# Kernel optimization log

Measured on AMD Instinct MI355X. Metric: run time of the kernel, lower is better.

The kernel has to match this reference:

```python
import jax, jax.numpy as jnp
import numpy as np

N, M, B, C, L, H = 8192, 8192, 16, 512, 64, 8
HEAD_DIM = C // H
PER_BATCH_KEYS = M // B
MASK_VAL = -1000.0  # matches torch masked_fill_ value


def setup_inputs() -> dict:
    key0 = jax.random.key(0)
    ks = jax.random.split(key0, 8)
    query = jax.random.normal(ks[0], (N, C), jnp.float32)
    key = jax.random.normal(ks[1], (M, C), jnp.float32)
    value = jax.random.normal(ks[2], (M, C), jnp.float32)
    # xavier-ish init for projections
    in_proj_weight = jax.random.normal(ks[3], (3 * C, C), jnp.float32) * (1.0 / np.sqrt(C))
    in_proj_bias = jnp.zeros((3 * C,), jnp.float32)
    out_w = jax.random.normal(ks[4], (C, C), jnp.float32) * (1.0 / np.sqrt(C))
    out_b = jnp.zeros((C,), jnp.float32)
    index_pair = jax.random.randint(ks[5], (N, L), 0, PER_BATCH_KEYS).astype(jnp.int32)
    pad = jax.random.uniform(ks[6], (N, L)) < 0.05
    index_pair = jnp.where(pad, jnp.int32(-1), index_pair)
    query_batch_cnt = jnp.full((B,), N // B, jnp.int32)
    key_batch_cnt = jnp.full((B,), PER_BATCH_KEYS, jnp.int32)
    index_pair_batch = jnp.repeat(jnp.arange(B, dtype=jnp.int32), N // B)
    return {
        "query": query, "key": key, "value": value,
        "in_proj_weight": in_proj_weight, "in_proj_bias": in_proj_bias,
        "out_w": out_w, "out_b": out_b,
        "index_pair": index_pair, "query_batch_cnt": query_batch_cnt,
        "key_batch_cnt": key_batch_cnt, "index_pair_batch": index_pair_batch,
    }


def reference(query, key, value, in_proj_weight, in_proj_bias, out_w, out_b,
              index_pair, query_batch_cnt, key_batch_cnt, index_pair_batch):
    embed_dim = query.shape[-1]
    scaling = float(HEAD_DIM) ** -0.5
    # qkv projections (in_proj_weight is [3C, C], applied as F.linear => x @ W.T + b)
    q = (query @ in_proj_weight[:embed_dim].T + in_proj_bias[:embed_dim]) * scaling
    k = key @ in_proj_weight[embed_dim:2 * embed_dim].T + in_proj_bias[embed_dim:2 * embed_dim]
    v = value @ in_proj_weight[2 * embed_dim:].T + in_proj_bias[2 * embed_dim:]
    q = q.reshape(N, H, HEAD_DIM)
    k = k.reshape(M, H, HEAD_DIM)
    v = v.reshape(M, H, HEAD_DIM)
    # local -> global key indices: offset by start of each query's batch key block
    key_start = jnp.cumsum(key_batch_cnt) - key_batch_cnt          # (B,)
    offset = key_start[index_pair_batch]                            # (N,)
    valid = index_pair >= 0                                         # (N, L)
    gidx = jnp.where(valid, index_pair + offset[:, None], 0)        # (N, L), safe gather
    # gather-based scores: (N, L, H)
    scores = jnp.einsum("nhd,nlhd->nlh", q, k[gidx])
    scores = jnp.where(valid[..., None], scores, MASK_VAL)
    w = jax.nn.softmax(scores, axis=1)                              # softmax over neighbors L
    # weighted value sum; masked weights underflow to exactly 0 in fp32
    attn = jnp.einsum("nlh,nlhd->nhd", w, v[gidx]).reshape(N, embed_dim)
    attn = attn @ out_w.T + out_b
    return attn, w.sum(axis=-1) / H
```

## Files before the change

### kernel.cpp

```cpp
#include <hip/hip_runtime.h>
#include <hip/hip_bf16.h>
#include <math.h>

#define NQ 8192
#define MK 8192
#define CD 512
#define LN 64
#define HH 8
#define HD 64
#define BB 16
#define KPB 512
#define QPB 512

typedef short short8 __attribute__((ext_vector_type(8)));
typedef float floatx4 __attribute__((ext_vector_type(4)));

__device__ __forceinline__ unsigned short f2bf(float x) {
    unsigned int u = __builtin_bit_cast(unsigned int, x);
    return (unsigned short)((u + 0x7FFFu + ((u >> 16) & 1u)) >> 16);
}
__device__ __forceinline__ unsigned int pkbf(float lo, float hi) {
    float2 f; f.x = lo; f.y = hi;
    __hip_bfloat162 h2 = __float22bfloat162_rn(f);
    unsigned int u;
    __builtin_memcpy(&u, &h2, 4);
    return u;
}
__device__ __forceinline__ float bflo(unsigned int u) {
    return __builtin_bit_cast(float, u << 16);
}
__device__ __forceinline__ float bfhij(unsigned int u) {
    return __builtin_bit_cast(float, u);
}
__device__ __forceinline__ short8 u4s8(uint4 u) {
    short8 s; __builtin_memcpy(&s, &u, 16); return s;
}
__device__ __forceinline__ float exp2v(float x) {
    float r; asm("v_exp_f32 %0, %1" : "=v"(r) : "v"(x)); return r;
}
__device__ __forceinline__ float rcpv(float x) {
    float r; asm("v_rcp_f32 %0, %1" : "=v"(r) : "v"(x)); return r;
}

__device__ __forceinline__ void gl_lds16(const unsigned short* g, unsigned short* l) {
    __builtin_amdgcn_global_load_lds(
        (const __attribute__((address_space(1))) unsigned int*)g,
        (__attribute__((address_space(3))) unsigned int*)l, 16, 0, 0);
}

struct ConvSeg { const float* src; unsigned short* dst; int n4; };
struct ConvArgs { ConvSeg s[5]; };

__global__ __launch_bounds__(256) void convert_bf16(ConvArgs a) {
    const int seg = blockIdx.y;
    const int i = blockIdx.x * 256 + threadIdx.x;
    if (i >= a.s[seg].n4) return;
    const float4 v = ((const float4*)a.s[seg].src)[i];
    uint2 o; o.x = pkbf(v.x, v.y); o.y = pkbf(v.z, v.w);
    ((uint2*)a.s[seg].dst)[i] = o;
}

template<int MI>
__device__ __forceinline__ void gemm_bf_body(const unsigned short* __restrict__ A,
                                             const unsigned short* __restrict__ W,
                                             const float* __restrict__ bias,
                                             float* __restrict__ outf,
                                             unsigned short* __restrict__ outb,
                                             float scale) {
    __shared__ unsigned short As[MI * 16 * 64];
    __shared__ unsigned short Bs[128 * 64];

    const int tid  = threadIdx.x;
    const int row0 = blockIdx.x * (MI * 16);
    const int col0 = blockIdx.y * 128;

    const int w    = tid >> 6;
    const int lane = tid & 63;
    const int q    = lane >> 4;
    const int ml   = lane & 15;

    const int sr = lane >> 3;
    const int sg = (lane & 7) ^ sr;
    const unsigned short* Ap = A + (size_t)(row0 + w * (MI * 4) + sr) * CD + sg * 8;
    const unsigned short* Wp = W + (size_t)(col0 + w * 32 + sr) * CD + sg * 8;
    unsigned short* Asw = &As[(w * (MI * 4)) * 64];
    unsigned short* Bsw = &Bs[(w * 32) * 64];

    floatx4 acc[MI][2];
#pragma unroll
    for (int i = 0; i < MI; ++i)
#pragma unroll
        for (int j = 0; j < 2; ++j)
            acc[i][j] = (floatx4){0.f, 0.f, 0.f, 0.f};

    for (int k0 = 0; k0 < CD; k0 += 64) {
        __syncthreads();
#pragma unroll
        for (int i = 0; i < MI / 2; ++i)
            gl_lds16(Ap + (size_t)(i * 8) * CD + k0, Asw + i * 8 * 64);
#pragma unroll
        for (int i = 0; i < 4; ++i)
            gl_lds16(Wp + (size_t)(i * 8) * CD + k0, Bsw + i * 8 * 64);
        __syncthreads();

#pragma unroll
        for (int kw = 0; kw < 2; ++kw) {
            short8 af[MI], bf[2];
            const int gp = ((kw * 4 + q) ^ (ml & 7)) * 8;
#pragma unroll
            for (int mi = 0; mi < MI; ++mi)
                af[mi] = *(const short8*)&As[(mi * 16 + ml) * 64 + gp];
#pragma unroll
            for (int ni = 0; ni < 2; ++ni)
                bf[ni] = *(const short8*)&Bs[(w * 32 + ni * 16 + ml) * 64 + gp];
#pragma unroll
            for (int mi = 0; mi < MI; ++mi)
#pragma unroll
                for (int ni = 0; ni < 2; ++ni)
                    acc[mi][ni] = __builtin_amdgcn_mfma_f32_16x16x32_bf16(
                        af[mi], bf[ni], acc[mi][ni], 0, 0, 0);
        }
    }

    float bv[2];
#pragma unroll
    for (int ni = 0; ni < 2; ++ni)
        bv[ni] = bias[col0 + w * 32 + ni * 16 + ml];
#pragma unroll
    for (int mi = 0; mi < MI; ++mi) {
#pragma unroll
        for (int ni = 0; ni < 2; ++ni) {
            const int cg = col0 + w * 32 + ni * 16 + ml;
#pragma unroll
            for (int rr = 0; rr < 4; ++rr) {
                const int rg = row0 + mi * 16 + q * 4 + rr;
                const float val = (acc[mi][ni][rr] + bv[ni]) * scale;
                if (outb) outb[(size_t)rg * CD + cg] = f2bf(val);
                else      outf[(size_t)rg * CD + cg] = val;
            }
        }
    }
}

#define QSCALE 0.18033688011112042f

__global__ __launch_bounds__(256, 3) void qkv_gemm(const unsigned short* __restrict__ A_bf,
                                                   const unsigned short* __restrict__ w_bf,
                                                   const float* __restrict__ bias,
                                                   unsigned short* __restrict__ q_bf,
                                                   unsigned short* __restrict__ k_bf,
                                                   unsigned short* __restrict__ v_bf) {
    const int z = blockIdx.z;
    const unsigned short* A = A_bf + (size_t)z * NQ * CD;
    unsigned short* outb = (z == 0) ? q_bf : ((z == 1) ? k_bf : v_bf);
    gemm_bf_body<8>(A, w_bf + (size_t)z * CD * CD, bias + (size_t)z * CD,
                    nullptr, outb, (z == 0) ? QSCALE : 1.0f);
}

__global__ __launch_bounds__(256) void out_gemm(const unsigned short* __restrict__ A,
                                                const unsigned short* __restrict__ W,
                                                const float* __restrict__ bias,
                                                float* __restrict__ out,
                                                const float* __restrict__ W8,
                                                float* __restrict__ out2) {
    if (blockIdx.y == 4) {
        const size_t base = (size_t)blockIdx.x * 4096 + threadIdx.x;
#pragma unroll
        for (int t = 0; t < 16; ++t) {
            const size_t i = base + (size_t)t * 256;
            float s = 0.f;
#pragma unroll
            for (int h = 0; h < HH; ++h) s += W8[(size_t)h * NQ * LN + i];
            out2[i] = s;
        }
        return;
    }
    gemm_bf_body<4>(A, W, bias, out, nullptr, 1.0f);
}

#define MFMA16(a, b, c) __builtin_amdgcn_mfma_f32_16x16x32_bf16(a, b, c, 0, 0, 0)
#define MK_ -1000.0f


#define FMA8(u, wgt) do {                                                     \
    const float w_ = (wgt);                                                   \
    a0 = fmaf(w_, bflo((u).x),  a0);  a1 = fmaf(w_, bfhij((u).x), a1);        \
    a2 = fmaf(w_, bflo((u).y),  a2);  a3 = fmaf(w_, bfhij((u).y), a3);        \
    a4 = fmaf(w_, bflo((u).z),  a4);  a5 = fmaf(w_, bfhij((u).z), a5);        \
    a6 = fmaf(w_, bflo((u).w),  a6);  a7 = fmaf(w_, bfhij((u).w), a7);        \
} while (0)

#define KRD(row, ch) (*(const uint4*)&K_s[(row) * 64 + ((((ch) ^ ((row) & 7))) * 8)])
#define VRD(row, ch) (*(const uint4*)&V_s[(row) * 64 + ((((ch) ^ ((row) & 7))) * 8)])

__global__ __launch_bounds__(512, 2) void attn_kernel(
    const unsigned short* __restrict__ q_bf,
    const unsigned short* __restrict__ k_bf,
    const unsigned short* __restrict__ v_bf,
    const int* __restrict__ index_pair,
    const int* __restrict__ key_batch_cnt,
    unsigned short* __restrict__ attn_bf,
    float* __restrict__ W8) {
    const int tid  = threadIdx.x;
    const int wid  = tid >> 6;
    const int lane = tid & 63;
    const int bid  = blockIdx.x;
    const int pair = bid & 127;
    const int qt   = bid >> 7;
    const int head = pair & 7;
    const int batch= pair >> 3;

    const int quad = lane >> 4, ml = lane & 15;
    const int r8 = lane >> 3, c8 = lane & 7;

    __shared__ unsigned short K_s[KPB * 64];
    __shared__ unsigned short V_s[KPB * 64];
    __shared__ int   g_s[8 * 64];
    __shared__ float w_st[8 * 64];
    __shared__ float red_s[8 * 64 * 9];

    int cnt = (lane < BB) ? key_batch_cnt[lane] : 0;
#pragma unroll
    for (int d = 1; d < BB; d <<= 1) {
        const int t = __shfl_up(cnt, d, 64);
        if (lane >= d) cnt += t;
    }
    const int off0 = (batch > 0) ? __shfl(cnt, batch - 1, 64) : 0;

#pragma unroll
    for (int j = 0; j < 8; ++j) {
        const int rowb = wid * 64 + j * 8;
        const size_t grow = (size_t)(off0 + rowb + r8);
        gl_lds16(k_bf + grow * CD + head * HD + ((c8 ^ r8) * 8), &K_s[rowb * 64]);
        gl_lds16(v_bf + grow * CD + head * HD + ((c8 ^ r8) * 8), &V_s[rowb * 64]);
    }
    __syncthreads();

    const int n0 = batch * QPB + qt * 128 + wid * 16;
    const bool p0 = ml & 1, p1 = ml & 2, p2 = ml & 4, p3 = ml & 8;
    const int jpub = (ml >> 2) * 16 + quad * 4 + (ml & 3);
    int*   gs  = &g_s[wid * 64];
    float* wst = &w_st[wid * 64];
    float* red = &red_s[wid * 64 * 9];

    int idx = index_pair[(size_t)n0 * LN + lane];
    for (int qi = 0; qi < 16; ++qi) {
        const int n = n0 + qi;
        const int idx_next = (qi < 15) ? index_pair[(size_t)(n + 1) * LN + lane] : 0;

        const unsigned long long vmask = __ballot(idx >= 0);
        const int g = (idx >= 0) ? idx : 0;
        gs[lane] = g;

        const int krow0 = __shfl(g, ml, 64);
        const int krow1 = __shfl(g, 16 + ml, 64);
        const int krow2 = __shfl(g, 32 + ml, 64);
        const int krow3 = __shfl(g, 48 + ml, 64);

        const unsigned long long tb = vmask >> (quad * 4);
        const unsigned mybits =
            (unsigned)( (tb & 0xFull)
                      | (((tb >> 16) & 0xFull) << 4)
                      | (((tb >> 32) & 0xFull) << 8)
                      | (((tb >> 48) & 0xFull) << 12));
        const bool b0  = mybits & 1u,          b1  = (mybits >> 1) & 1u;
        const bool b2  = (mybits >> 2) & 1u,   b3  = (mybits >> 3) & 1u;
        const bool b4  = (mybits >> 4) & 1u,   b5  = (mybits >> 5) & 1u;
        const bool b6  = (mybits >> 6) & 1u,   b7  = (mybits >> 7) & 1u;
        const bool b8  = (mybits >> 8) & 1u,   b9  = (mybits >> 9) & 1u;
        const bool b10 = (mybits >> 10) & 1u,  b11 = (mybits >> 11) & 1u;
        const bool b12 = (mybits >> 12) & 1u,  b13 = (mybits >> 13) & 1u;
        const bool b14 = (mybits >> 14) & 1u,  b15 = (mybits >> 15) & 1u;

        const unsigned short* qrow = q_bf + (size_t)n * CD + head * HD;
        const uint4 qa0 = *(const uint4*)(qrow + quad * 8);
        const uint4 qa1 = *(const uint4*)(qrow + 32 + quad * 8);

        const uint4 kf00 = KRD(krow0, quad), kf01 = KRD(krow0, 4 + quad);
        const uint4 kf10 = KRD(krow1, quad), kf11 = KRD(krow1, 4 + quad);
        const uint4 kf20 = KRD(krow2, quad), kf21 = KRD(krow2, 4 + quad);
        const uint4 kf30 = KRD(krow3, quad), kf31 = KRD(krow3, 4 + quad);

        floatx4 z0 = (floatx4){0.f,0.f,0.f,0.f}, z1 = z0, z2 = z0, z3 = z0;
        z0 = MFMA16(u4s8(kf00), u4s8(qa0), z0);
        z0 = MFMA16(u4s8(kf01), u4s8(qa1), z0);
        z1 = MFMA16(u4s8(kf10), u4s8(qa0), z1);
        z1 = MFMA16(u4s8(kf11), u4s8(qa1), z1);
        z2 = MFMA16(u4s8(kf20), u4s8(qa0), z2);
        z2 = MFMA16(u4s8(kf21), u4s8(qa1), z2);
        z3 = MFMA16(u4s8(kf30), u4s8(qa0), z3);
        z3 = MFMA16(u4s8(kf31), u4s8(qa1), z3);

        float s00 = b0  ? z0[0] : MK_,  s01 = b1  ? z0[1] : MK_;
        float s02 = b2  ? z0[2] : MK_,  s03 = b3  ? z0[3] : MK_;
        float s04 = b4  ? z1[0] : MK_,  s05 = b5  ? z1[1] : MK_;
        float s06 = b6  ? z1[2] : MK_,  s07 = b7  ? z1[3] : MK_;
        float s08 = b8  ? z2[0] : MK_,  s09 = b9  ? z2[1] : MK_;
        float s10 = b10 ? z2[2] : MK_,  s11 = b11 ? z2[3] : MK_;
        float s12 = b12 ? z3[0] : MK_,  s13 = b13 ? z3[1] : MK_;
        float s14 = b14 ? z3[2] : MK_,  s15 = b15 ? z3[3] : MK_;
        float mx = fmaxf(fmaxf(fmaxf(fmaxf(s00, s01), fmaxf(s02, s03)),
                               fmaxf(fmaxf(s04, s05), fmaxf(s06, s07))),
                         fmaxf(fmaxf(fmaxf(s08, s09), fmaxf(s10, s11)),
                               fmaxf(fmaxf(s12, s13), fmaxf(s14, s15))));
        mx = fmaxf(mx, __shfl_xor(mx, 16, 64));
        mx = fmaxf(mx, __shfl_xor(mx, 32, 64));
        s00 = exp2v(s00 - mx); s01 = exp2v(s01 - mx);
        s02 = exp2v(s02 - mx); s03 = exp2v(s03 - mx);
        s04 = exp2v(s04 - mx); s05 = exp2v(s05 - mx);
        s06 = exp2v(s06 - mx); s07 = exp2v(s07 - mx);
        s08 = exp2v(s08 - mx); s09 = exp2v(s09 - mx);
        s10 = exp2v(s10 - mx); s11 = exp2v(s11 - mx);
        s12 = exp2v(s12 - mx); s13 = exp2v(s13 - mx);
        s14 = exp2v(s14 - mx); s15 = exp2v(s15 - mx);
        float sm = (((s00 + s01) + (s02 + s03)) + ((s04 + s05) + (s06 + s07)))
                 + (((s08 + s09) + (s10 + s11)) + ((s12 + s13) + (s14 + s15)));
        sm += __shfl_xor(sm, 16, 64);
        sm += __shfl_xor(sm, 32, 64);
        const float rs = rcpv(sm);
        const float t0 = p1 ? (p0 ? s03 : s02) : (p0 ? s01 : s00);
        const float t1 = p1 ? (p0 ? s07 : s06) : (p0 ? s05 : s04);
        const float t2 = p1 ? (p0 ? s11 : s10) : (p0 ? s09 : s08);
        const float t3 = p1 ? (p0 ? s15 : s14) : (p0 ? s13 : s12);
        const float pick = p3 ? (p2 ? t3 : t2) : (p2 ? t1 : t0);
        const float w = pick * rs;
        wst[jpub] = w;
        W8[((size_t)head * NQ + n) * LN + jpub] = w * 0.125f;

        const int   vr0 = gs[0 * 8 + r8], vr1 = gs[1 * 8 + r8];
        const int   vr2 = gs[2 * 8 + r8], vr3 = gs[3 * 8 + r8];
        const int   vr4 = gs[4 * 8 + r8], vr5 = gs[5 * 8 + r8];
        const int   vr6 = gs[6 * 8 + r8], vr7 = gs[7 * 8 + r8];
        const float wv0 = wst[0 * 8 + r8], wv1 = wst[1 * 8 + r8];
        const float wv2 = wst[2 * 8 + r8], wv3 = wst[3 * 8 + r8];
        const float wv4 = wst[4 * 8 + r8], wv5 = wst[5 * 8 + r8];
        const float wv6 = wst[6 * 8 + r8], wv7 = wst[7 * 8 + r8];
        const uint4 vv0 = VRD(vr0, c8);
        const uint4 vv1 = VRD(vr1, c8);
        const uint4 vv2 = VRD(vr2, c8);
        const uint4 vv3 = VRD(vr3, c8);
        const uint4 vv4 = VRD(vr4, c8);
        const uint4 vv5 = VRD(vr5, c8);
        const uint4 vv6 = VRD(vr6, c8);
        const uint4 vv7 = VRD(vr7, c8);
        float a0 = 0.f, a1 = 0.f, a2 = 0.f, a3 = 0.f;
        float a4 = 0.f, a5 = 0.f, a6 = 0.f, a7 = 0.f;
        FMA8(vv0, wv0); FMA8(vv1, wv1); FMA8(vv2, wv2); FMA8(vv3, wv3);
        FMA8(vv4, wv4); FMA8(vv5, wv5); FMA8(vv6, wv6); FMA8(vv7, wv7);

        red[lane * 9 + 0] = a0; red[lane * 9 + 1] = a1;
        red[lane * 9 + 2] = a2; red[lane * 9 + 3] = a3;
        red[lane * 9 + 4] = a4; red[lane * 9 + 5] = a5;
        red[lane * 9 + 6] = a6; red[lane * 9 + 7] = a7;
        const int bcol = lane >> 3, e = lane & 7;
        const float s = (((red[(0 * 8 + bcol) * 9 + e] + red[(1 * 8 + bcol) * 9 + e])
                        + (red[(2 * 8 + bcol) * 9 + e] + red[(3 * 8 + bcol) * 9 + e]))
                       + ((red[(4 * 8 + bcol) * 9 + e] + red[(5 * 8 + bcol) * 9 + e])
                        + (red[(6 * 8 + bcol) * 9 + e] + red[(7 * 8 + bcol) * 9 + e])));
        attn_bf[(size_t)n * CD + head * HD + lane] = f2bf(s);

        idx = idx_next;
    }
}

extern "C" void kernel_launch(void* const* d_in, const int* in_sizes, int n_in,
                              void* d_out, int out_size, void* d_ws, size_t ws_size,
                              hipStream_t stream) {
    const float* query   = (const float*)d_in[0];
    const float* key     = (const float*)d_in[1];
    const float* value   = (const float*)d_in[2];
    const float* ipw     = (const float*)d_in[3];
    const float* ipb     = (const float*)d_in[4];
    const float* out_w   = (const float*)d_in[5];
    const float* out_b   = (const float*)d_in[6];
    const int*   index_pair       = (const int*)d_in[7];
    const int*   key_batch_cnt    = (const int*)d_in[9];

    float* out = (float*)d_out;
    unsigned short* q_bf  = (unsigned short*)d_ws;
    unsigned short* k_bf  = q_bf + (size_t)NQ * CD;
    unsigned short* v_bf  = k_bf + (size_t)NQ * CD;
    unsigned short* A_bf  = v_bf + (size_t)NQ * CD;
    unsigned short* w_bf  = A_bf + (size_t)3 * NQ * CD;
    unsigned short* ow_bf = w_bf + (size_t)3 * CD * CD;
    unsigned short* attn_bf = A_bf;
    float* W8 = (float*)(A_bf + (size_t)NQ * CD);

    ConvArgs ca;
    ca.s[0] = {query, A_bf,                       NQ * CD / 4};
    ca.s[1] = {key,   A_bf + (size_t)NQ * CD,     NQ * CD / 4};
    ca.s[2] = {value, A_bf + (size_t)2 * NQ * CD, NQ * CD / 4};
    ca.s[3] = {ipw,   w_bf,                       3 * CD * CD / 4};
    ca.s[4] = {out_w, ow_bf,                      CD * CD / 4};
    dim3 g0(NQ * CD / 4 / 256, 5);
    convert_bf16<<<g0, 256, 0, stream>>>(ca);

    dim3 g1(NQ / 128, CD / 128, 3);
    qkv_gemm<<<g1, 256, 0, stream>>>(A_bf, w_bf, ipb, q_bf, k_bf, v_bf);

    attn_kernel<<<512, 512, 0, stream>>>(q_bf, k_bf, v_bf, index_pair,
                                         key_batch_cnt, attn_bf, W8);

    dim3 g3(NQ / 64, 5, 1);
    out_gemm<<<g3, 256, 0, stream>>>(attn_bf, ow_bf, out_b, out,
                                     W8, out + (size_t)NQ * CD);
}
```

Baseline: 199.1 us.

## Distribute softmax across lanes, unswizzle V tile, enlarge output GEMM tile

```diff
diff --git a/kernel.cpp b/kernel.cpp
--- a/kernel.cpp
+++ b/kernel.cpp
@@ -164,9 +164,9 @@
                                                 const float* __restrict__ W8,
                                                 float* __restrict__ out2) {
     if (blockIdx.y == 4) {
-        const size_t base = (size_t)blockIdx.x * 4096 + threadIdx.x;
-#pragma unroll
-        for (int t = 0; t < 16; ++t) {
+        const size_t base = (size_t)blockIdx.x * 8192 + threadIdx.x;
+#pragma unroll
+        for (int t = 0; t < 32; ++t) {
             const size_t i = base + (size_t)t * 256;
             float s = 0.f;
 #pragma unroll
@@ -175,7 +175,7 @@
         }
         return;
     }
-    gemm_bf_body<4>(A, W, bias, out, nullptr, 1.0f);
+    gemm_bf_body<8>(A, W, bias, out, nullptr, 1.0f);
 }
 
 #define MFMA16(a, b, c) __builtin_amdgcn_mfma_f32_16x16x32_bf16(a, b, c, 0, 0, 0)
@@ -191,7 +191,6 @@
 } while (0)
 
 #define KRD(row, ch) (*(const uint4*)&K_s[(row) * 64 + ((((ch) ^ ((row) & 7))) * 8)])
-#define VRD(row, ch) (*(const uint4*)&V_s[(row) * 64 + ((((ch) ^ ((row) & 7))) * 8)])
 
 __global__ __launch_bounds__(512, 2) void attn_kernel(
     const unsigned short* __restrict__ q_bf,
@@ -232,13 +231,16 @@
         const int rowb = wid * 64 + j * 8;
         const size_t grow = (size_t)(off0 + rowb + r8);
         gl_lds16(k_bf + grow * CD + head * HD + ((c8 ^ r8) * 8), &K_s[rowb * 64]);
-        gl_lds16(v_bf + grow * CD + head * HD + ((c8 ^ r8) * 8), &V_s[rowb * 64]);
+        gl_lds16(v_bf + grow * CD + head * HD + (c8 * 8),        &V_s[rowb * 64]);
     }
     __syncthreads();
 
     const int n0 = batch * QPB + qt * 128 + wid * 16;
-    const bool p0 = ml & 1, p1 = ml & 2, p2 = ml & 4, p3 = ml & 8;
-    const int jpub = (ml >> 2) * 16 + quad * 4 + (ml & 3);
+    const int grp_own = ml >> 2;
+    const bool gs0 = ml & 4, gs1 = ml & 8;
+    const bool rs0 = ml & 1, rs1 = ml & 2;
+    const int jpub = grp_own * 16 + quad * 4 + (ml & 3);
+    const int nibsh = grp_own * 16 + quad * 4;
     int*   gs  = &g_s[wid * 64];
     float* wst = &w_st[wid * 64];
     float* red = &red_s[wid * 64 * 9];
@@ -256,21 +258,6 @@
         const int krow1 = __shfl(g, 16 + ml, 64);
         const int krow2 = __shfl(g, 32 + ml, 64);
         const int krow3 = __shfl(g, 48 + ml, 64);
-
-        const unsigned long long tb = vmask >> (quad * 4);
-        const unsigned mybits =
-            (unsigned)( (tb & 0xFull)
-                      | (((tb >> 16) & 0xFull) << 4)
-                      | (((tb >> 32) & 0xFull) << 8)
-                      | (((tb >> 48) & 0xFull) << 12));
-        const bool b0  = mybits & 1u,          b1  = (mybits >> 1) & 1u;
-        const bool b2  = (mybits >> 2) & 1u,   b3  = (mybits >> 3) & 1u;
-        const bool b4  = (mybits >> 4) & 1u,   b5  = (mybits >> 5) & 1u;
-        const bool b6  = (mybits >> 6) & 1u,   b7  = (mybits >> 7) & 1u;
-        const bool b8  = (mybits >> 8) & 1u,   b9  = (mybits >> 9) & 1u;
-        const bool b10 = (mybits >> 10) & 1u,  b11 = (mybits >> 11) & 1u;
-        const bool b12 = (mybits >> 12) & 1u,  b13 = (mybits >> 13) & 1u;
-        const bool b14 = (mybits >> 14) & 1u,  b15 = (mybits >> 15) & 1u;
 
         const unsigned short* qrow = q_bf + (size_t)n * CD + head * HD;
         const uint4 qa0 = *(const uint4*)(qrow + quad * 8);
@@ -291,38 +278,29 @@
         z3 = MFMA16(u4s8(kf30), u4s8(qa0), z3);
         z3 = MFMA16(u4s8(kf31), u4s8(qa1), z3);
 
-        float s00 = b0  ? z0[0] : MK_,  s01 = b1  ? z0[1] : MK_;
-        float s02 = b2  ? z0[2] : MK_,  s03 = b3  ? z0[3] : MK_;
-        float s04 = b4  ? z1[0] : MK_,  s05 = b5  ? z1[1] : MK_;
-        float s06 = b6  ? z1[2] : MK_,  s07 = b7  ? z1[3] : MK_;
-        float s08 = b8  ? z2[0] : MK_,  s09 = b9  ? z2[1] : MK_;
-        float s10 = b10 ? z2[2] : MK_,  s11 = b11 ? z2[3] : MK_;
-        float s12 = b12 ? z3[0] : MK_,  s13 = b13 ? z3[1] : MK_;
-        float s14 = b14 ? z3[2] : MK_,  s15 = b15 ? z3[3] : MK_;
-        float mx = fmaxf(fmaxf(fmaxf(fmaxf(s00, s01), fmaxf(s02, s03)),
-                               fmaxf(fmaxf(s04, s05), fmaxf(s06, s07))),
-                         fmaxf(fmaxf(fmaxf(s08, s09), fmaxf(s10, s11)),
-                               fmaxf(fmaxf(s12, s13), fmaxf(s14, s15))));
+        float s0 = gs1 ? (gs0 ? z3[0] : z2[0]) : (gs0 ? z1[0] : z0[0]);
+        float s1 = gs1 ? (gs0 ? z3[1] : z2[1]) : (gs0 ? z1[1] : z0[1]);
+        float s2 = gs1 ? (gs0 ? z3[2] : z2[2]) : (gs0 ? z1[2] : z0[2]);
+        float s3 = gs1 ? (gs0 ? z3[3] : z2[3]) : (gs0 ? z1[3] : z0[3]);
+        const unsigned nib = (unsigned)((vmask >> nibsh) & 0xFull);
+        s0 = (nib & 1u) ? s0 : MK_;
+        s1 = (nib & 2u) ? s1 : MK_;
+        s2 = (nib & 4u) ? s2 : MK_;
+        s3 = (nib & 8u) ? s3 : MK_;
+        float mx = fmaxf(fmaxf(s0, s1), fmaxf(s2, s3));
+        mx = fmaxf(mx, __shfl_xor(mx, 4, 64));
+        mx = fmaxf(mx, __shfl_xor(mx, 8, 64));
         mx = fmaxf(mx, __shfl_xor(mx, 16, 64));
         mx = fmaxf(mx, __shfl_xor(mx, 32, 64));
-        s00 = exp2v(s00 - mx); s01 = exp2v(s01 - mx);
-        s02 = exp2v(s02 - mx); s03 = exp2v(s03 - mx);
-        s04 = exp2v(s04 - mx); s05 = exp2v(s05 - mx);
-        s06 = exp2v(s06 - mx); s07 = exp2v(s07 - mx);
-        s08 = exp2v(s08 - mx); s09 = exp2v(s09 - mx);
-        s10 = exp2v(s10 - mx); s11 = exp2v(s11 - mx);
-        s12 = exp2v(s12 - mx); s13 = exp2v(s13 - mx);
-        s14 = exp2v(s14 - mx); s15 = exp2v(s15 - mx);
-        float sm = (((s00 + s01) + (s02 + s03)) + ((s04 + s05) + (s06 + s07)))
-                 + (((s08 + s09) + (s10 + s11)) + ((s12 + s13) + (s14 + s15)));
+        const float e0 = exp2v(s0 - mx), e1 = exp2v(s1 - mx);
+        const float e2 = exp2v(s2 - mx), e3 = exp2v(s3 - mx);
+        float sm = (e0 + e1) + (e2 + e3);
+        sm += __shfl_xor(sm, 4, 64);
+        sm += __shfl_xor(sm, 8, 64);
         sm += __shfl_xor(sm, 16, 64);
         sm += __shfl_xor(sm, 32, 64);
         const float rs = rcpv(sm);
-        const float t0 = p1 ? (p0 ? s03 : s02) : (p0 ? s01 : s00);
-        const float t1 = p1 ? (p0 ? s07 : s06) : (p0 ? s05 : s04);
-        const float t2 = p1 ? (p0 ? s11 : s10) : (p0 ? s09 : s08);
-        const float t3 = p1 ? (p0 ? s15 : s14) : (p0 ? s13 : s12);
-        const float pick = p3 ? (p2 ? t3 : t2) : (p2 ? t1 : t0);
+        const float pick = rs1 ? (rs0 ? e3 : e2) : (rs0 ? e1 : e0);
         const float w = pick * rs;
         wst[jpub] = w;
         W8[((size_t)head * NQ + n) * LN + jpub] = w * 0.125f;
@@ -335,14 +313,14 @@
         const float wv2 = wst[2 * 8 + r8], wv3 = wst[3 * 8 + r8];
         const float wv4 = wst[4 * 8 + r8], wv5 = wst[5 * 8 + r8];
         const float wv6 = wst[6 * 8 + r8], wv7 = wst[7 * 8 + r8];
-        const uint4 vv0 = VRD(vr0, c8);
-        const uint4 vv1 = VRD(vr1, c8);
-        const uint4 vv2 = VRD(vr2, c8);
-        const uint4 vv3 = VRD(vr3, c8);
-        const uint4 vv4 = VRD(vr4, c8);
-        const uint4 vv5 = VRD(vr5, c8);
-        const uint4 vv6 = VRD(vr6, c8);
-        const uint4 vv7 = VRD(vr7, c8);
+        const uint4 vv0 = *(const uint4*)&V_s[vr0 * 64 + c8 * 8];
+        const uint4 vv1 = *(const uint4*)&V_s[vr1 * 64 + c8 * 8];
+        const uint4 vv2 = *(const uint4*)&V_s[vr2 * 64 + c8 * 8];
+        const uint4 vv3 = *(const uint4*)&V_s[vr3 * 64 + c8 * 8];
+        const uint4 vv4 = *(const uint4*)&V_s[vr4 * 64 + c8 * 8];
+        const uint4 vv5 = *(const uint4*)&V_s[vr5 * 64 + c8 * 8];
+        const uint4 vv6 = *(const uint4*)&V_s[vr6 * 64 + c8 * 8];
+        const uint4 vv7 = *(const uint4*)&V_s[vr7 * 64 + c8 * 8];
         float a0 = 0.f, a1 = 0.f, a2 = 0.f, a3 = 0.f;
         float a4 = 0.f, a5 = 0.f, a6 = 0.f, a7 = 0.f;
         FMA8(vv0, wv0); FMA8(vv1, wv1); FMA8(vv2, wv2); FMA8(vv3, wv3);
@@ -401,7 +379,7 @@
     attn_kernel<<<512, 512, 0, stream>>>(q_bf, k_bf, v_bf, index_pair,
                                          key_batch_cnt, attn_bf, W8);
 
-    dim3 g3(NQ / 64, 5, 1);
+    dim3 g3(NQ / 128, 5, 1);
     out_gemm<<<g3, 256, 0, stream>>>(attn_bf, ow_bf, out_b, out,
                                      W8, out + (size_t)NQ * CD);
 }
```

Measured after the change: 197.6 us. About the same (-0.8%).
